# Kernel tuning notes

Measured on AMD Instinct MI355X. Metric: run time of the kernel, lower is better.

Reference implementation:

```python
import jax, jax.numpy as jnp
import numpy as np


def setup_inputs() -> dict:
    key = jax.random.key(0)
    ks = jax.random.split(key, 8)
    N, DIN, DOUT = 8192, 1024, 1024
    s = 1.0 / np.sqrt(DIN)
    return {
        "gAB": jax.random.normal(ks[0], (N, DIN), dtype=jnp.float32),
        "gAG": jax.random.normal(ks[1], (N, DIN), dtype=jnp.float32),
        "Wab": jax.random.normal(ks[2], (DIN, DOUT), dtype=jnp.float32) * s,
        "Wag": jax.random.normal(ks[3], (DIN, DOUT), dtype=jnp.float32) * s,
        "bab": jax.random.normal(ks[4], (DOUT,), dtype=jnp.float32) * 0.01,
        "bag": jax.random.normal(ks[5], (DOUT,), dtype=jnp.float32) * 0.01,
        "sAB": jax.random.normal(ks[6], (N, DOUT), dtype=jnp.float32),
        "sAG": jax.random.normal(ks[7], (N, DOUT), dtype=jnp.float32),
    }


def reference(gAB, gAG, Wab, Wag, bab, bag, sAB, sAG) -> jnp.ndarray:
    # project() per encoder (Linear): [N, DIN] @ [DIN, DOUT] + b
    pAB = gAB @ Wab + bab  # [N, DOUT]
    pAG = gAG @ Wag + bag  # [N, DOUT]
    # torch.diag(pAB @ pAG.T) == row-wise dot product (avoids O(N^2 d) waste)
    h1 = jnp.sum(pAB * pAG, axis=1, keepdims=True)  # [N, 1]
    h2 = jnp.sum(sAB * sAG, axis=1, keepdims=True)  # [N, 1]
    # mean over concatenated (h1, h2) columns, keepdim=True
    h = jnp.mean(jnp.concatenate([h1, h2], axis=1), axis=1, keepdims=True)  # [N, 1]
    return h
```

## Files before the change

### kernel.cpp

```cpp
#include <hip/hip_runtime.h>
#include <hip/hip_bf16.h>
#include <stdint.h>

typedef __attribute__((ext_vector_type(8))) short bf16x8;
typedef __attribute__((ext_vector_type(4))) float f32x4;

#define DIN 1024
#define NROWS 8192

__device__ __forceinline__ unsigned short f2bf(float f) {
    union { float f; unsigned u; } v; v.f = f;
    unsigned r = v.u + 0x7FFFu + ((v.u >> 16) & 1u);
    return (unsigned short)(r >> 16);
}

__device__ __forceinline__ int fswz(int r) { return (r ^ (r >> 2)) & 3; }

__device__ __forceinline__ size_t swz_byte(int R, int col) {
    return ((size_t)R * DIN + (col & ~31)) * 2 + (size_t)((((col >> 3) & 3) ^ fswz(R)) << 4) + (size_t)((col & 7) * 2);
}

__device__ __forceinline__ void gload_lds16(const void* g, void* l) {
    __builtin_amdgcn_global_load_lds(
        (const __attribute__((address_space(1))) unsigned*)g,
        (__attribute__((address_space(3))) unsigned*)l, 16, 0, 0);
}

__global__ __launch_bounds__(256) void prep_kernel(const float* __restrict__ Wab,
                                                   const float* __restrict__ Wag,
                                                   const float* __restrict__ bab,
                                                   const float* __restrict__ bag,
                                                   float* __restrict__ ws_f,
                                                   unsigned short* __restrict__ Whab,
                                                   unsigned short* __restrict__ Whag) {
    int b = blockIdx.x;
    int wave = threadIdx.x >> 6, lane = threadIdx.x & 63;
    if (b == 256) {
        if (wave == 0) {
            float acc = 0.f;
            for (int j = lane; j < DIN; j += 64) acc += bab[j] * bag[j];
            for (int off = 32; off; off >>= 1) acc += __shfl_xor(acc, off);
            if (lane == 0) ws_f[2048] = acc;
        }
        return;
    }
    int r = b * 4 + wave;
    int fr = fswz(r);
    {
        const float* wrow = Wab + (size_t)r * DIN;
        char* hrow = (char*)Whab + (size_t)r * DIN * 2;
        float acc = 0.f;
#pragma unroll
        for (int it = 0; it < 4; ++it) {
            int col = it * 256 + lane * 4;
            float4 w = *reinterpret_cast<const float4*>(wrow + col);
            float4 bv = *reinterpret_cast<const float4*>(bag + col);
            acc += w.x * bv.x + w.y * bv.y + w.z * bv.z + w.w * bv.w;
            ushort4 h; h.x = f2bf(w.x); h.y = f2bf(w.y); h.z = f2bf(w.z); h.w = f2bf(w.w);
            *reinterpret_cast<ushort4*>(hrow + (col & ~31) * 2 + ((((col >> 3) & 3) ^ fr) << 4) + (col & 7) * 2) = h;
        }
        for (int off = 32; off; off >>= 1) acc += __shfl_xor(acc, off);
        if (lane == 0) ws_f[r] = acc;
    }
    {
        const float* wrow = Wag + (size_t)r * DIN;
        char* hrow = (char*)Whag + (size_t)r * DIN * 2;
        float acc = 0.f;
#pragma unroll
        for (int it = 0; it < 4; ++it) {
            int col = it * 256 + lane * 4;
            float4 w = *reinterpret_cast<const float4*>(wrow + col);
            float4 bv = *reinterpret_cast<const float4*>(bab + col);
            acc += w.x * bv.x + w.y * bv.y + w.z * bv.z + w.w * bv.w;
            ushort4 h; h.x = f2bf(w.x); h.y = f2bf(w.y); h.z = f2bf(w.z); h.w = f2bf(w.w);
            *reinterpret_cast<ushort4*>(hrow + (col & ~31) * 2 + ((((col >> 3) & 3) ^ fr) << 4) + (col & 7) * 2) = h;
        }
        for (int off = 32; off; off >>= 1) acc += __shfl_xor(acc, off);
        if (lane == 0) ws_f[1024 + r] = acc;
    }
}

__global__ __launch_bounds__(512) void mt_kernel(const unsigned short* __restrict__ Whag,
                                                 const unsigned short* __restrict__ Whab,
                                                 unsigned short* __restrict__ Mt) {
    __shared__ unsigned short sm[2][2][2][2048];
    int tid = threadIdx.x;
    int wave = tid >> 6, grp = wave >> 2, w4 = wave & 3;
    int lane = tid & 63, kg = lane >> 4, cl = lane & 15;
    int wr = w4 >> 1, wc = w4 & 1;
    int br = blockIdx.x >> 4, bc = blockIdx.x & 15;
    int u = tid & 255, urow = u >> 2, uchunk = u & 3;

    const char* Abase = (const char*)Whag + ((size_t)(br * 64 + urow) * DIN + grp * 512) * 2 + uchunk * 16;
    const char* Bbase = (const char*)Whab + ((size_t)(bc * 64 + urow) * DIN + grp * 512) * 2 + uchunk * 16;

    int offA[2], offB[2];
#pragma unroll
    for (int m = 0; m < 2; ++m) { int row = wr * 32 + m * 16 + cl; offA[m] = row * 32 + ((kg ^ fswz(row)) << 3); }
#pragma unroll
    for (int n = 0; n < 2; ++n) { int row = wc * 32 + n * 16 + cl; offB[n] = row * 32 + ((kg ^ fswz(row)) << 3); }

    f32x4 acc[2][2] = {};
    gload_lds16(Abase, &sm[grp][0][0][u * 8]);
    gload_lds16(Bbase, &sm[grp][0][1][u * 8]);
    __syncthreads();
    for (int t = 0; t < 16; ++t) {
        int p = t & 1;
        if (t < 15) {
            gload_lds16(Abase + (t + 1) * 64, &sm[grp][p ^ 1][0][u * 8]);
            gload_lds16(Bbase + (t + 1) * 64, &sm[grp][p ^ 1][1][u * 8]);
        }
        bf16x8 af[2], bfr[2];
#pragma unroll
        for (int m = 0; m < 2; ++m) af[m] = *reinterpret_cast<const bf16x8*>(&sm[grp][p][0][offA[m]]);
#pragma unroll
        for (int n = 0; n < 2; ++n) bfr[n] = *reinterpret_cast<const bf16x8*>(&sm[grp][p][1][offB[n]]);
#pragma unroll
        for (int m = 0; m < 2; ++m)
#pragma unroll
            for (int n = 0; n < 2; ++n)
                acc[m][n] = __builtin_amdgcn_mfma_f32_16x16x32_bf16(af[m], bfr[n], acc[m][n], 0, 0, 0);
        __syncthreads();
    }
    float* red = (float*)sm;
    if (grp == 1) {
#pragma unroll
        for (int m = 0; m < 2; ++m)
#pragma unroll
            for (int n = 0; n < 2; ++n)
#pragma unroll
                for (int j = 0; j < 4; ++j)
                    red[(wr * 32 + m * 16 + kg * 4 + j) * 68 + wc * 32 + n * 16 + cl] = acc[m][n][j];
    }
    __syncthreads();
    if (grp == 0) {
#pragma unroll
        for (int m = 0; m < 2; ++m)
#pragma unroll
            for (int n = 0; n < 2; ++n)
#pragma unroll
                for (int j = 0; j < 4; ++j) {
                    int rl = wr * 32 + m * 16 + kg * 4 + j, cll = wc * 32 + n * 16 + cl;
                    float v = acc[m][n][j] + red[rl * 68 + cll];
                    int R = br * 64 + rl, C = bc * 64 + cll;
                    *(unsigned short*)((char*)Mt + swz_byte(R, C & ~3) + (C & 3) * 2) = f2bf(v);
                }
    }
}

__global__ __launch_bounds__(256) void stream_kernel(const float* __restrict__ gAB,
                                                     const float* __restrict__ sAB,
                                                     const float* __restrict__ sAG,
                                                     const float* __restrict__ ws_f,
                                                     unsigned short* __restrict__ gABh,
                                                     float* __restrict__ out,
                                                     int writecast) {
    int wave = threadIdx.x >> 6, lane = threadIdx.x & 63;
    int row = blockIdx.x * 4 + wave;
    const float* ga = gAB + (size_t)row * DIN;
    const float* sa = sAB + (size_t)row * DIN;
    const float* sg = sAG + (size_t)row * DIN;
    char* gh = (char*)gABh + (size_t)row * DIN * 2;
    int fr = fswz(row);
    float acc = 0.f;
#pragma unroll
    for (int cc = 0; cc < 4; ++cc) {
        int col = cc * 256 + lane * 4;
        float4 a = *reinterpret_cast<const float4*>(ga + col);
        float4 x = *reinterpret_cast<const float4*>(sa + col);
        float4 y = *reinterpret_cast<const float4*>(sg + col);
        float4 v = *reinterpret_cast<const float4*>(ws_f + col);
        acc += x.x * y.x + x.y * y.y + x.z * y.z + x.w * y.w;
        acc += a.x * v.x + a.y * v.y + a.z * v.z + a.w * v.w;
        if (writecast) {
            ushort4 h; h.x = f2bf(a.x); h.y = f2bf(a.y); h.z = f2bf(a.z); h.w = f2bf(a.w);
            *reinterpret_cast<ushort4*>(gh + (col & ~31) * 2 + ((((col >> 3) & 3) ^ fr) << 4) + (col & 7) * 2) = h;
        }
    }
#pragma unroll
    for (int off = 32; off; off >>= 1) acc += __shfl_xor(acc, off);
    if (lane == 0) out[row] = 0.5f * (acc + ws_f[2048]);
}

template <int PRECAST, int KSPLIT>
__global__ __launch_bounds__(256, 4) void gemm_kernel(const float* __restrict__ gAB,
                                                      const unsigned short* __restrict__ gABh,
                                                      const float* __restrict__ gAG,
                                                      const unsigned short* __restrict__ Mt,
                                                      const float* __restrict__ ws_f,
                                                      float* __restrict__ out) {
    __shared__ unsigned short lds_a[2][128 * 32];
    __shared__ unsigned short lds_b[2][128 * 32];
    constexpr int KLEN = DIN / KSPLIT;
    constexpr int NSTEP = KLEN / 32;
    int b = blockIdx.x;
    int x = b & 7, s = b >> 3;
    int rblk = x + 8 * (s & 7);
    int u2 = s >> 3;
    int ks = u2 & (KSPLIT - 1);
    int cblk = u2 / KSPLIT;
    int tid = threadIdx.x, wave = tid >> 6, lane = tid & 63;
    int wr = wave >> 1, wc = wave & 1;
    int kg = lane >> 4, cl = lane & 15;
    int row0 = rblk * 128, col0 = cblk * 128;

    int offA[4], offB[4];
#pragma unroll
    for (int m = 0; m < 4; ++m) { int row = wr * 64 + m * 16 + cl; offA[m] = row * 32 + ((kg ^ fswz(row)) << 3); }
#pragma unroll
    for (int n = 0; n < 4; ++n) { int row = wc * 64 + n * 16 + cl; offB[n] = row * 32 + ((kg ^ fswz(row)) << 3); }

    size_t kofs = (size_t)(ks * KLEN) * 2;
    const char* Ab = (const char*)gABh + (size_t)row0 * DIN * 2 + kofs;
    const char* Bb = (const char*)Mt + (size_t)col0 * DIN * 2 + kofs;
    int u0 = tid, u1 = tid + 256;
    size_t a0 = (size_t)(u0 >> 2) * (DIN * 2) + (u0 & 3) * 16;
    size_t a1 = (size_t)(u1 >> 2) * (DIN * 2) + (u1 & 3) * 16;

    f32x4 acc[4][4] = {};
    float4 ra[4];
    if (PRECAST) {
        gload_lds16(Ab + a0, (char*)&lds_a[0][0] + u0 * 16);
        gload_lds16(Ab + a1, (char*)&lds_a[0][0] + u1 * 16);
    } else {
#pragma unroll
        for (int it = 0; it < 4; ++it) {
            int u = tid + it * 256;
            ra[it] = *reinterpret_cast<const float4*>(gAB + (size_t)(row0 + (u >> 3)) * DIN + ks * KLEN + (u & 7) * 4);
        }
#pragma unroll
        for (int it = 0; it < 4; ++it) {
            int u = tid + it * 256, row = u >> 3, c4 = u & 7;
            ushort4 h; h.x = f2bf(ra[it].x); h.y = f2bf(ra[it].y); h.z = f2bf(ra[it].z); h.w = f2bf(ra[it].w);
            *reinterpret_cast<ushort4*>((char*)&lds_a[0][0] + row * 64 + ((((c4 >> 1) ^ fswz(row))) << 4) + (c4 & 1) * 8) = h;
        }
    }
    gload_lds16(Bb + a0, (char*)&lds_b[0][0] + u0 * 16);
    gload_lds16(Bb + a1, (char*)&lds_b[0][0] + u1 * 16);
    __syncthreads();

    for (int t = 0; t < NSTEP; ++t) {
        int p = t & 1;
        if (t < NSTEP - 1) {
            if (PRECAST) {
                gload_lds16(Ab + a0 + (t + 1) * 64, (char*)&lds_a[p ^ 1][0] + u0 * 16);
                gload_lds16(Ab + a1 + (t + 1) * 64, (char*)&lds_a[p ^ 1][0] + u1 * 16);
            } else {
#pragma unroll
                for (int it = 0; it < 4; ++it) {
                    int u = tid + it * 256;
                    ra[it] = *reinterpret_cast<const float4*>(gAB + (size_t)(row0 + (u >> 3)) * DIN + ks * KLEN + (t + 1) * 32 + (u & 7) * 4);
                }
            }
            gload_lds16(Bb + a0 + (t + 1) * 64, (char*)&lds_b[p ^ 1][0] + u0 * 16);
            gload_lds16(Bb + a1 + (t + 1) * 64, (char*)&lds_b[p ^ 1][0] + u1 * 16);
        }
        bf16x8 af[4], bfr[4];
#pragma unroll
        for (int m = 0; m < 4; ++m) af[m] = *reinterpret_cast<const bf16x8*>(&lds_a[p][offA[m]]);
#pragma unroll
        for (int n = 0; n < 4; ++n) bfr[n] = *reinterpret_cast<const bf16x8*>(&lds_b[p][offB[n]]);
#pragma unroll
        for (int m = 0; m < 4; ++m)
#pragma unroll
            for (int n = 0; n < 4; ++n)
                acc[m][n] = __builtin_amdgcn_mfma_f32_16x16x32_bf16(af[m], bfr[n], acc[m][n], 0, 0, 0);
        if (!PRECAST && t < NSTEP - 1) {
#pragma unroll
            for (int it = 0; it < 4; ++it) {
                int u = tid + it * 256, row = u >> 3, c4 = u & 7;
                ushort4 h; h.x = f2bf(ra[it].x); h.y = f2bf(ra[it].y); h.z = f2bf(ra[it].z); h.w = f2bf(ra[it].w);
                *reinterpret_cast<ushort4*>((char*)&lds_a[p ^ 1][0] + row * 64 + ((((c4 >> 1) ^ fswz(row))) << 4) + (c4 & 1) * 8) = h;
            }
        }
        __syncthreads();
    }

    const float* vag = ws_f + 1024;
#pragma unroll
    for (int m = 0; m < 4; ++m)
#pragma unroll
        for (int j = 0; j < 4; ++j) {
            int row = row0 + wr * 64 + m * 16 + kg * 4 + j;
            const float* gr = gAG + (size_t)row * DIN;
            float t = 0.f;
#pragma unroll
            for (int n = 0; n < 4; ++n) {
                int col = col0 + wc * 64 + n * 16 + cl;
                float addv = (ks == 0) ? vag[col] : 0.f;
                t += gr[col] * (acc[m][n][j] + addv);
            }
            t += __shfl_xor(t, 1);
            t += __shfl_xor(t, 2);
            t += __shfl_xor(t, 4);
            t += __shfl_xor(t, 8);
            if (cl == 0) atomicAdd(out + row, 0.5f * t);
        }
}

extern "C" void kernel_launch(void* const* d_in, const int* in_sizes, int n_in,
                              void* d_out, int out_size, void* d_ws, size_t ws_size,
                              hipStream_t stream) {
    const float* gAB = (const float*)d_in[0];
    const float* gAG = (const float*)d_in[1];
    const float* Wab = (const float*)d_in[2];
    const float* Wag = (const float*)d_in[3];
    const float* bab = (const float*)d_in[4];
    const float* bag = (const float*)d_in[5];
    const float* sAB = (const float*)d_in[6];
    const float* sAG = (const float*)d_in[7];
    float* out = (float*)d_out;

    float* ws_f = (float*)d_ws;
    char* base = (char*)d_ws + 16384;
    unsigned short* Mt = (unsigned short*)base;
    unsigned short* Whag = (unsigned short*)(base + (size_t)2 * 1024 * 1024);
    unsigned short* Whab = (unsigned short*)(base + (size_t)4 * 1024 * 1024);
    unsigned short* gABh = (unsigned short*)(base + (size_t)6 * 1024 * 1024);
    size_t need_full = 16384 + (size_t)22 * 1024 * 1024;
    int precast = (ws_size >= need_full) ? 1 : 0;

    prep_kernel<<<257, 256, 0, stream>>>(Wab, Wag, bab, bag, ws_f, Whab, Whag);
    mt_kernel<<<256, 512, 0, stream>>>(Whag, Whab, Mt);
    stream_kernel<<<2048, 256, 0, stream>>>(gAB, sAB, sAG, ws_f, gABh, out, precast);
    if (precast)
        gemm_kernel<1, 2><<<1024, 256, 0, stream>>>(gAB, gABh, gAG, Mt, ws_f, out);
    else
        gemm_kernel<0, 1><<<512, 256, 0, stream>>>(gAB, gABh, gAG, Mt, ws_f, out);
}
```

Before: 67.16 us.

## Fuse streaming dot products and fp32 cast into split-K GEMM epilogue

Removes the separate stream kernel that computed the sAB·sAG and gAB·vab row dots and wrote a bf16 copy of gAB. The GEMM now reads fp32 gAB directly and casts it to bf16 in registers before writing to LDS, using split-K of 2. The extra row-dot terms are added in the epilogue of the ks==0 blocks, and the output is zeroed with a memset. This saves one launch and one pass that wrote and re-read a bf16 gAB buffer. In exchange the GEMM does more global fp32 loads and register conversion per step, and the epilogue does scattered strided reads of sAB and sAG.

```diff
diff --git a/kernel.cpp b/kernel.cpp
--- a/kernel.cpp
+++ b/kernel.cpp
@@ -148,47 +148,14 @@
     }
 }
 
-__global__ __launch_bounds__(256) void stream_kernel(const float* __restrict__ gAB,
+template <int KSPLIT>
+__global__ __launch_bounds__(256, 4) void gemm_fused(const float* __restrict__ gAB,
+                                                     const float* __restrict__ gAG,
                                                      const float* __restrict__ sAB,
                                                      const float* __restrict__ sAG,
+                                                     const unsigned short* __restrict__ Mt,
                                                      const float* __restrict__ ws_f,
-                                                     unsigned short* __restrict__ gABh,
-                                                     float* __restrict__ out,
-                                                     int writecast) {
-    int wave = threadIdx.x >> 6, lane = threadIdx.x & 63;
-    int row = blockIdx.x * 4 + wave;
-    const float* ga = gAB + (size_t)row * DIN;
-    const float* sa = sAB + (size_t)row * DIN;
-    const float* sg = sAG + (size_t)row * DIN;
-    char* gh = (char*)gABh + (size_t)row * DIN * 2;
-    int fr = fswz(row);
-    float acc = 0.f;
-#pragma unroll
-    for (int cc = 0; cc < 4; ++cc) {
-        int col = cc * 256 + lane * 4;
-        float4 a = *reinterpret_cast<const float4*>(ga + col);
-        float4 x = *reinterpret_cast<const float4*>(sa + col);
-        float4 y = *reinterpret_cast<const float4*>(sg + col);
-        float4 v = *reinterpret_cast<const float4*>(ws_f + col);
-        acc += x.x * y.x + x.y * y.y + x.z * y.z + x.w * y.w;
-        acc += a.x * v.x + a.y * v.y + a.z * v.z + a.w * v.w;
-        if (writecast) {
-            ushort4 h; h.x = f2bf(a.x); h.y = f2bf(a.y); h.z = f2bf(a.z); h.w = f2bf(a.w);
-            *reinterpret_cast<ushort4*>(gh + (col & ~31) * 2 + ((((col >> 3) & 3) ^ fr) << 4) + (col & 7) * 2) = h;
-        }
-    }
-#pragma unroll
-    for (int off = 32; off; off >>= 1) acc += __shfl_xor(acc, off);
-    if (lane == 0) out[row] = 0.5f * (acc + ws_f[2048]);
-}
-
-template <int PRECAST, int KSPLIT>
-__global__ __launch_bounds__(256, 4) void gemm_kernel(const float* __restrict__ gAB,
-                                                      const unsigned short* __restrict__ gABh,
-                                                      const float* __restrict__ gAG,
-                                                      const unsigned short* __restrict__ Mt,
-                                                      const float* __restrict__ ws_f,
-                                                      float* __restrict__ out) {
+                                                     float* __restrict__ out) {
     __shared__ unsigned short lds_a[2][128 * 32];
     __shared__ unsigned short lds_b[2][128 * 32];
     constexpr int KLEN = DIN / KSPLIT;
@@ -210,50 +177,41 @@
 #pragma unroll
     for (int n = 0; n < 4; ++n) { int row = wc * 64 + n * 16 + cl; offB[n] = row * 32 + ((kg ^ fswz(row)) << 3); }
 
-    size_t kofs = (size_t)(ks * KLEN) * 2;
-    const char* Ab = (const char*)gABh + (size_t)row0 * DIN * 2 + kofs;
-    const char* Bb = (const char*)Mt + (size_t)col0 * DIN * 2 + kofs;
+    size_t kofs = (size_t)(ks * KLEN);
+    const char* Bb = (const char*)Mt + ((size_t)col0 * DIN + kofs) * 2;
     int u0 = tid, u1 = tid + 256;
-    size_t a0 = (size_t)(u0 >> 2) * (DIN * 2) + (u0 & 3) * 16;
-    size_t a1 = (size_t)(u1 >> 2) * (DIN * 2) + (u1 & 3) * 16;
+    size_t b0 = (size_t)(u0 >> 2) * (DIN * 2) + (u0 & 3) * 16;
+    size_t b1 = (size_t)(u1 >> 2) * (DIN * 2) + (u1 & 3) * 16;
+    const float* Abase = gAB + (size_t)row0 * DIN + kofs;
 
     f32x4 acc[4][4] = {};
     float4 ra[4];
-    if (PRECAST) {
-        gload_lds16(Ab + a0, (char*)&lds_a[0][0] + u0 * 16);
-        gload_lds16(Ab + a1, (char*)&lds_a[0][0] + u1 * 16);
-    } else {
-#pragma unroll
-        for (int it = 0; it < 4; ++it) {
-            int u = tid + it * 256;
-            ra[it] = *reinterpret_cast<const float4*>(gAB + (size_t)(row0 + (u >> 3)) * DIN + ks * KLEN + (u & 7) * 4);
-        }
-#pragma unroll
-        for (int it = 0; it < 4; ++it) {
-            int u = tid + it * 256, row = u >> 3, c4 = u & 7;
-            ushort4 h; h.x = f2bf(ra[it].x); h.y = f2bf(ra[it].y); h.z = f2bf(ra[it].z); h.w = f2bf(ra[it].w);
-            *reinterpret_cast<ushort4*>((char*)&lds_a[0][0] + row * 64 + ((((c4 >> 1) ^ fswz(row))) << 4) + (c4 & 1) * 8) = h;
-        }
-    }
-    gload_lds16(Bb + a0, (char*)&lds_b[0][0] + u0 * 16);
-    gload_lds16(Bb + a1, (char*)&lds_b[0][0] + u1 * 16);
+
+    gload_lds16(Bb + b0, (char*)&lds_b[0][0] + u0 * 16);
+    gload_lds16(Bb + b1, (char*)&lds_b[0][0] + u1 * 16);
+#pragma unroll
+    for (int it = 0; it < 4; ++it) {
+        int u = tid + it * 256;
+        ra[it] = *reinterpret_cast<const float4*>(Abase + (size_t)(u >> 3) * DIN + (u & 7) * 4);
+    }
+#pragma unroll
+    for (int it = 0; it < 4; ++it) {
+        int u = tid + it * 256, row = u >> 3, c4 = u & 7;
+        ushort4 h; h.x = f2bf(ra[it].x); h.y = f2bf(ra[it].y); h.z = f2bf(ra[it].z); h.w = f2bf(ra[it].w);
+        *reinterpret_cast<ushort4*>((char*)&lds_a[0][0] + row * 64 + ((((c4 >> 1) ^ fswz(row))) << 4) + (c4 & 1) * 8) = h;
+    }
     __syncthreads();
 
     for (int t = 0; t < NSTEP; ++t) {
         int p = t & 1;
         if (t < NSTEP - 1) {
-            if (PRECAST) {
-                gload_lds16(Ab + a0 + (t + 1) * 64, (char*)&lds_a[p ^ 1][0] + u0 * 16);
-                gload_lds16(Ab + a1 + (t + 1) * 64, (char*)&lds_a[p ^ 1][0] + u1 * 16);
-            } else {
-#pragma unroll
-                for (int it = 0; it < 4; ++it) {
-                    int u = tid + it * 256;
-                    ra[it] = *reinterpret_cast<const float4*>(gAB + (size_t)(row0 + (u >> 3)) * DIN + ks * KLEN + (t + 1) * 32 + (u & 7) * 4);
-                }
-            }
-            gload_lds16(Bb + a0 + (t + 1) * 64, (char*)&lds_b[p ^ 1][0] + u0 * 16);
-            gload_lds16(Bb + a1 + (t + 1) * 64, (char*)&lds_b[p ^ 1][0] + u1 * 16);
+#pragma unroll
+            for (int it = 0; it < 4; ++it) {
+                int u = tid + it * 256;
+                ra[it] = *reinterpret_cast<const float4*>(Abase + (size_t)(u >> 3) * DIN + (t + 1) * 32 + (u & 7) * 4);
+            }
+            gload_lds16(Bb + b0 + (t + 1) * 64, (char*)&lds_b[p ^ 1][0] + u0 * 16);
+            gload_lds16(Bb + b1 + (t + 1) * 64, (char*)&lds_b[p ^ 1][0] + u1 * 16);
         }
         bf16x8 af[4], bfr[4];
 #pragma unroll
@@ -265,7 +223,7 @@
 #pragma unroll
             for (int n = 0; n < 4; ++n)
                 acc[m][n] = __builtin_amdgcn_mfma_f32_16x16x32_bf16(af[m], bfr[n], acc[m][n], 0, 0, 0);
-        if (!PRECAST && t < NSTEP - 1) {
+        if (t < NSTEP - 1) {
 #pragma unroll
             for (int it = 0; it < 4; ++it) {
                 int u = tid + it * 256, row = u >> 3, c4 = u & 7;
@@ -276,7 +234,9 @@
         __syncthreads();
     }
 
+    const float* vab = ws_f;
     const float* vag = ws_f + 1024;
+    float cbias = ws_f[2048];
 #pragma unroll
     for (int m = 0; m < 4; ++m)
 #pragma unroll
@@ -290,11 +250,24 @@
                 float addv = (ks == 0) ? vag[col] : 0.f;
                 t += gr[col] * (acc[m][n][j] + addv);
             }
+            if (ks == 0) {
+                const float* gar = gAB + (size_t)row * DIN;
+                const float* sar = sAB + (size_t)row * DIN;
+                const float* sgr = sAG + (size_t)row * DIN;
+#pragma unroll
+                for (int n = 0; n < 4; ++n) {
+                    int col = col0 + wc * 64 + n * 16 + cl;
+                    t += gar[col] * vab[col] + sar[col] * sgr[col];
+                }
+            }
             t += __shfl_xor(t, 1);
             t += __shfl_xor(t, 2);
             t += __shfl_xor(t, 4);
             t += __shfl_xor(t, 8);
-            if (cl == 0) atomicAdd(out + row, 0.5f * t);
+            if (cl == 0) {
+                float add = (ks == 0 && cblk == 0 && wc == 0) ? cbias : 0.f;
+                atomicAdd(out + row, 0.5f * (t + add));
+            }
         }
 }
 
@@ -316,15 +289,9 @@
     unsigned short* Mt = (unsigned short*)base;
     unsigned short* Whag = (unsigned short*)(base + (size_t)2 * 1024 * 1024);
     unsigned short* Whab = (unsigned short*)(base + (size_t)4 * 1024 * 1024);
-    unsigned short* gABh = (unsigned short*)(base + (size_t)6 * 1024 * 1024);
-    size_t need_full = 16384 + (size_t)22 * 1024 * 1024;
-    int precast = (ws_size >= need_full) ? 1 : 0;
-
+
+    hipMemsetAsync(d_out, 0, (size_t)out_size * sizeof(float), stream);
     prep_kernel<<<257, 256, 0, stream>>>(Wab, Wag, bab, bag, ws_f, Whab, Whag);
     mt_kernel<<<256, 512, 0, stream>>>(Whag, Whab, Mt);
-    stream_kernel<<<2048, 256, 0, stream>>>(gAB, sAB, sAG, ws_f, gABh, out, precast);
-    if (precast)
-        gemm_kernel<1, 2><<<1024, 256, 0, stream>>>(gAB, gABh, gAG, Mt, ws_f, out);
-    else
-        gemm_kernel<0, 1><<<512, 256, 0, stream>>>(gAB, gABh, gAG, Mt, ws_f, out);
-}
+    gemm_fused<2><<<1024, 256, 0, stream>>>(gAB, gAG, sAB, sAG, Mt, ws_f, out);
+}
```

Result: slower. 70.45 us (+4.9%).
